# Optimization experiments

Hardware: AMD Instinct MI355X
Metric: run time of the kernel (lower is better)

The kernel has to match this reference:

```python
import jax, jax.numpy as jnp
import numpy as np
from jax import lax

B, C, H, W = 8, 128, 64, 64


def conv1x1(x, w):
    # x: [B, Cin, H, W], w: [Cout, Cin] (1x1 conv, no bias)
    return jnp.einsum('oc,bchw->bohw', w, x)


def maxpool2x2(x):
    # 2x2 max pool, stride 2, NCHW
    return lax.reduce_window(x, -jnp.inf, lax.max, (1, 1, 2, 2), (1, 1, 2, 2), 'VALID')


def setup_inputs() -> dict:
    key = jax.random.key(0)
    ks = jax.random.split(key, 5)
    c8, c2 = C // 8, C // 2
    inputs = jax.random.normal(ks[0], (B, C, H, W), dtype=jnp.float32)
    w_theta = jax.random.normal(ks[1], (c8, C), dtype=jnp.float32) * (1.0 / np.sqrt(C))
    w_phi = jax.random.normal(ks[2], (c8, C), dtype=jnp.float32) * (1.0 / np.sqrt(C))
    w_g = jax.random.normal(ks[3], (c2, C), dtype=jnp.float32) * (1.0 / np.sqrt(C))
    w_o = jax.random.normal(ks[4], (C, c2), dtype=jnp.float32) * (1.0 / np.sqrt(c2))
    gamma = jnp.float32(0.1)  # nonzero so attention branch contributes
    return {"inputs": inputs, "w_theta": w_theta, "w_phi": w_phi,
            "w_g": w_g, "w_o": w_o, "gamma": gamma}


def reference(inputs, w_theta, w_phi, w_g, w_o, gamma):
    batch, c, h, w = inputs.shape
    c8, c2 = c // 8, c // 2
    theta = conv1x1(inputs, w_theta).reshape(batch, c8, h * w)            # [B, C/8, HW]
    phi = maxpool2x2(conv1x1(inputs, w_phi)).reshape(batch, c8, -1)       # [B, C/8, HW/4]
    g = maxpool2x2(conv1x1(inputs, w_g)).reshape(batch, c2, -1)           # [B, C/2, HW/4]
    # beta[b, i, j] = softmax_j( theta[b,:,i] . phi[b,:,j] )
    scores = jnp.einsum('bci,bcj->bij', theta, phi)                       # [B, HW, HW/4]
    beta = jax.nn.softmax(scores, axis=-1)
    o = jnp.einsum('bcj,bij->bci', g, beta).reshape(batch, c2, h, w)      # [B, C/2, H, W]
    o = conv1x1(o, w_o)                                                   # [B, C, H, W]
    return gamma * o + inputs
```

## Files before the change

kernel.cpp:

```cpp
#include <hip/hip_runtime.h>
#include <math.h>

#define HW 4096
#define SHIFT 12.0f

typedef __attribute__((ext_vector_type(4)))  short short4v;
typedef __attribute__((ext_vector_type(8)))  short short8;
typedef __attribute__((ext_vector_type(4)))  float f32x4;
typedef __attribute__((ext_vector_type(16))) float f32x16;
typedef __attribute__((ext_vector_type(4)))  int   int4v;

#define MFMA16 __builtin_amdgcn_mfma_f32_16x16x32_bf16
#define MFMA32 __builtin_amdgcn_mfma_f32_32x32x16_bf16

__device__ inline short f2b(float f) {
    union { float f; unsigned u; } v; v.f = f;
    unsigned r = v.u + 0x7fffu + ((v.u >> 16) & 1u);
    return (short)(r >> 16);
}
__device__ inline int pk2(float a, float b) {
    return (int)((unsigned)(unsigned short)f2b(a) |
                 ((unsigned)(unsigned short)f2b(b) << 16));
}
__device__ inline short8 ld8(const float* p) {
    f32x4 a = *(const f32x4*)p;
    f32x4 b = *(const f32x4*)(p + 4);
    short8 r;
    r[0] = f2b(a.x); r[1] = f2b(a.y); r[2] = f2b(a.z); r[3] = f2b(a.w);
    r[4] = f2b(b.x); r[5] = f2b(b.y); r[6] = f2b(b.z); r[7] = f2b(b.w);
    return r;
}
__device__ inline float max4(float a, float b, float c, float d) {
    return fmaxf(fmaxf(a, b), fmaxf(c, d));
}

__global__ __launch_bounds__(256) void conv_pool(
    const float* __restrict__ x, const float* __restrict__ wt,
    const float* __restrict__ wp, const float* __restrict__ wg,
    short* __restrict__ theta_t, short* __restrict__ phi_t,
    short* __restrict__ g_blk)
{
    __shared__ __align__(16) short xl[128 * 68];
    const int tid = threadIdx.x;
    const int w = tid >> 6, lane = tid & 63, l15 = lane & 15, lg = (lane >> 4) & 3;
    const int bid = blockIdx.x;
    const int b = bid >> 6, ri = bid & 63, rp = ri >> 1, h = ri & 1;
    const float* xb = x + (size_t)b * 128 * HW + rp * 128 + h * 32;

    for (int it = 0; it < 8; it++) {
        int idx = it * 256 + tid;
        int c = idx >> 4, q = idx & 15;
        int px4 = q * 4, r = px4 >> 5, col4 = px4 & 31;
        f32x4 v = *(const f32x4*)(xb + (size_t)c * HW + r * 64 + col4);
        short4v sv = { f2b(v.x), f2b(v.y), f2b(v.z), f2b(v.w) };
        *(short4v*)(xl + c * 68 + px4) = sv;
    }
    __syncthreads();

    const int p = w & 1, csbase = (w >> 1) * 3;
    f32x4 acc[2][3];
#pragma unroll
    for (int cc = 0; cc < 2; cc++)
#pragma unroll
        for (int cl = 0; cl < 3; cl++) acc[cc][cl] = (f32x4){0.f, 0.f, 0.f, 0.f};

#pragma unroll
    for (int ks = 0; ks < 4; ks++) {
        short8 a[2];
#pragma unroll
        for (int cc = 0; cc < 2; cc++) {
            int px = (p + 2 * cc) * 16 + l15;
#pragma unroll
            for (int q = 0; q < 8; q++)
                a[cc][q] = xl[(ks * 32 + lg * 8 + q) * 68 + px];
        }
#pragma unroll
        for (int csl = 0; csl < 3; csl++) {
            int cs = csbase + csl;
            const float* wrow;
            if (cs == 0)      wrow = wt + l15 * 128;
            else if (cs == 1) wrow = wp + l15 * 128;
            else              wrow = wg + ((cs - 2) * 16 + l15) * 128;
            short8 bf = ld8(wrow + ks * 32 + lg * 8);
            acc[0][csl] = MFMA16(a[0], bf, acc[0][csl], 0, 0, 0);
            acc[1][csl] = MFMA16(a[1], bf, acc[1][csl], 0, 0, 0);
        }
    }

    const size_t pixb = (size_t)b * 4096 + rp * 128 + h * 32 + p * 16;
#pragma unroll
    for (int csl = 0; csl < 3; csl++) {
        int cs = csbase + csl;
        if (cs == 0) {
#pragma unroll
            for (int cc = 0; cc < 2; cc++)
#pragma unroll
                for (int r = 0; r < 4; r++)
                    theta_t[(pixb + cc * 64 + lg * 4 + r) * 16 + l15] =
                        f2b(acc[cc][csl][r]);
        } else if (cs == 1) {
#pragma unroll
            for (int h2 = 0; h2 < 2; h2++) {
                float m = max4(acc[0][csl][2 * h2], acc[0][csl][2 * h2 + 1],
                               acc[1][csl][2 * h2], acc[1][csl][2 * h2 + 1]);
                int j = rp * 32 + h * 16 + p * 8 + lg * 2 + h2;
                phi_t[((size_t)b * 1024 + j) * 16 + l15] = f2b(m);
            }
        } else {
            int gcrow = (cs - 2) * 16 + l15;
            float m0 = max4(acc[0][csl][0], acc[0][csl][1], acc[1][csl][0], acc[1][csl][1]);
            float m1 = max4(acc[0][csl][2], acc[0][csl][3], acc[1][csl][2], acc[1][csl][3]);
            int jb = rp * 2 + h, jl = p * 8 + lg * 2;
            *(int*)(g_blk + (((size_t)b * 64 + jb) * 64 + gcrow) * 16 + jl) = pk2(m0, m1);
        }
    }
}

__global__ __launch_bounds__(256) void attn_k(
    const float* __restrict__ x, const short* __restrict__ theta_t,
    const short* __restrict__ phi_t, const short* __restrict__ g_blk,
    const float* __restrict__ wo, const float* __restrict__ gamma_p,
    float* __restrict__ out)
{
    __shared__ float lds[4 * 2 * 16 * 64 + 4 * 64];
    const int tid = threadIdx.x;
    const int w = tid >> 6, lane = tid & 63, l31 = lane & 31, lam = lane >> 5;
    const int b = blockIdx.x >> 7, i0 = (blockIdx.x & 127) << 5;
    const int i = i0 + l31;

    short8 tb = *(const short8*)(theta_t + ((size_t)b * 4096 + i) * 16 + lam * 8);

    f32x16 acc0, acc1, z16;
#pragma unroll
    for (int r = 0; r < 16; r++) { acc0[r] = 0.f; acc1[r] = 0.f; z16[r] = 0.f; }
    float rs = 0.f;

    for (int t = 0; t < 4; t++) {
        const int jt = w * 4 + t;
        f32x16 s0, s1;
        {
            short8 pa0 = *(const short8*)(phi_t + ((size_t)b * 1024 + jt * 64 + l31) * 16 + lam * 8);
            short8 pa1 = *(const short8*)(phi_t + ((size_t)b * 1024 + jt * 64 + 32 + l31) * 16 + lam * 8);
            s0 = MFMA32(pa0, tb, z16, 0, 0, 0);
            s1 = MFMA32(pa1, tb, z16, 0, 0, 0);
        }
        int W[16], X[16];
#pragma unroll
        for (int jk = 0; jk < 2; jk++)
#pragma unroll
            for (int rg = 0; rg < 4; rg++)
#pragma unroll
                for (int h = 0; h < 2; h++) {
                    float p0 = __expf((jk ? s1 : s0)[rg * 4 + 2 * h]     - SHIFT);
                    float p1 = __expf((jk ? s1 : s0)[rg * 4 + 2 * h + 1] - SHIFT);
                    rs += p0 + p1;
                    W[jk * 8 + rg * 2 + h] = pk2(p0, p1);
                }
#pragma unroll
        for (int k = 0; k < 16; k++) X[k] = __shfl_xor(W[k], 32, 64);

#pragma unroll
        for (int ck = 0; ck < 4; ck++) {
            const int cb2 = (ck >> 1) * 8 + (ck & 1) * 4;
            int4v pi;
            pi.x = lam ? X[cb2 + 2] : W[cb2];
            pi.y = lam ? X[cb2 + 3] : W[cb2 + 1];
            pi.z = lam ? W[cb2 + 2] : X[cb2];
            pi.w = lam ? W[cb2 + 3] : X[cb2 + 1];
            short8 pb = __builtin_bit_cast(short8, pi);
            const short* gp = g_blk + (((size_t)b * 64 + jt * 4 + ck) * 64) * 16;
            short8 ga0 = *(const short8*)(gp + (l31)      * 16 + lam * 8);
            short8 ga1 = *(const short8*)(gp + (32 + l31) * 16 + lam * 8);
            acc0 = MFMA32(ga0, pb, acc0, 0, 0, 0);
            acc1 = MFMA32(ga1, pb, acc1, 0, 0, 0);
        }
    }

    rs += __shfl_xor(rs, 32, 64);

#pragma unroll
    for (int reg = 0; reg < 16; reg++) {
        lds[((w * 2 + 0) * 16 + reg) * 64 + lane] = acc0[reg];
        lds[((w * 2 + 1) * 16 + reg) * 64 + lane] = acc1[reg];
    }
    lds[8192 + w * 64 + lane] = rs;
    __syncthreads();

    float o[32];
#pragma unroll
    for (int cs2 = 0; cs2 < 2; cs2++)
#pragma unroll
        for (int reg = 0; reg < 16; reg++)
            o[cs2 * 16 + reg] =
                (lds[((0 * 2 + cs2) * 16 + reg) * 64 + lane] +
                 lds[((1 * 2 + cs2) * 16 + reg) * 64 + lane]) +
                (lds[((2 * 2 + cs2) * 16 + reg) * 64 + lane] +
                 lds[((3 * 2 + cs2) * 16 + reg) * 64 + lane]);
    float lf = (lds[8192 + 0 * 64 + lane] + lds[8192 + 1 * 64 + lane]) +
               (lds[8192 + 2 * 64 + lane] + lds[8192 + 3 * 64 + lane]);
    float rinv = 1.0f / lf;
#pragma unroll
    for (int k = 0; k < 32; k++) o[k] *= rinv;

    int Wo[16], Xo[16];
#pragma unroll
    for (int cs2 = 0; cs2 < 2; cs2++)
#pragma unroll
        for (int rg = 0; rg < 4; rg++)
#pragma unroll
            for (int h = 0; h < 2; h++)
                Wo[cs2 * 8 + rg * 2 + h] =
                    pk2(o[cs2 * 16 + rg * 4 + 2 * h], o[cs2 * 16 + rg * 4 + 2 * h + 1]);
#pragma unroll
    for (int k = 0; k < 16; k++) Xo[k] = __shfl_xor(Wo[k], 32, 64);

    const float gam = gamma_p[0];
    f32x16 oc;
#pragma unroll
    for (int r = 0; r < 16; r++) oc[r] = 0.f;
#pragma unroll
    for (int kc = 0; kc < 4; kc++) {
        const int cb2 = (kc >> 1) * 8 + (kc & 1) * 4;
        int4v pi;
        pi.x = lam ? Xo[cb2 + 2] : Wo[cb2];
        pi.y = lam ? Xo[cb2 + 3] : Wo[cb2 + 1];
        pi.z = lam ? Wo[cb2 + 2] : Xo[cb2];
        pi.w = lam ? Wo[cb2 + 3] : Xo[cb2 + 1];
        short8 ob = __builtin_bit_cast(short8, pi);
        short8 wa = ld8(wo + (size_t)(w * 32 + l31) * 64 + kc * 16 + lam * 8);
        oc = MFMA32(wa, ob, oc, 0, 0, 0);
    }
#pragma unroll
    for (int reg = 0; reg < 16; reg++) {
        int co = w * 32 + (reg & 3) + 8 * (reg >> 2) + 4 * lam;
        size_t idx = ((size_t)b * 128 + co) * HW + i0 + l31;
        out[idx] = gam * oc[reg] + x[idx];
    }
}

extern "C" void kernel_launch(void* const* d_in, const int* in_sizes, int n_in,
                              void* d_out, int out_size, void* d_ws, size_t ws_size,
                              hipStream_t stream)
{
    const float* x     = (const float*)d_in[0];
    const float* wt    = (const float*)d_in[1];
    const float* wp    = (const float*)d_in[2];
    const float* wg    = (const float*)d_in[3];
    const float* wo    = (const float*)d_in[4];
    const float* gamma = (const float*)d_in[5];
    float* out = (float*)d_out;

    char* ws = (char*)d_ws;
    short* theta_t = (short*)(ws + 0);
    short* phi_t   = (short*)(ws + 1048576);
    short* g_blk   = (short*)(ws + 1310720);

    conv_pool<<<512,  256, 0, stream>>>(x, wt, wp, wg, theta_t, phi_t, g_blk);
    attn_k   <<<1024, 256, 0, stream>>>(x, theta_t, phi_t, g_blk, wo, gamma, out);
}
```

Before: 102.9 us.

## Pre-convert weights to bf16 and use hardware pack and permlane swap instructions

Adds a small kernel that converts all four weight matrices to bf16 once per call, so the conv and attention kernels load bf16 weights directly instead of converting floats per lane. The software bf16 rounding is replaced with the v_cvt_pk_bf16_f32 instruction, and the xor-32 shuffles plus lane selects are replaced with v_permlane32_swap. The softmax shift is folded into the MFMA accumulator initial value, which removes a subtract per exponential. This costs an extra kernel launch and a workspace buffer for the converted weights.

```diff
diff --git a/kernel.cpp b/kernel.cpp
--- a/kernel.cpp
+++ b/kernel.cpp
@@ -6,9 +6,10 @@
 
 typedef __attribute__((ext_vector_type(4)))  short short4v;
 typedef __attribute__((ext_vector_type(8)))  short short8;
+typedef __attribute__((ext_vector_type(2)))  int   int2v;
+typedef __attribute__((ext_vector_type(4)))  int   int4v;
 typedef __attribute__((ext_vector_type(4)))  float f32x4;
 typedef __attribute__((ext_vector_type(16))) float f32x16;
-typedef __attribute__((ext_vector_type(4)))  int   int4v;
 
 #define MFMA16 __builtin_amdgcn_mfma_f32_16x16x32_bf16
 #define MFMA32 __builtin_amdgcn_mfma_f32_32x32x16_bf16
@@ -18,25 +19,36 @@
     unsigned r = v.u + 0x7fffu + ((v.u >> 16) & 1u);
     return (short)(r >> 16);
 }
-__device__ inline int pk2(float a, float b) {
-    return (int)((unsigned)(unsigned short)f2b(a) |
-                 ((unsigned)(unsigned short)f2b(b) << 16));
-}
-__device__ inline short8 ld8(const float* p) {
-    f32x4 a = *(const f32x4*)p;
-    f32x4 b = *(const f32x4*)(p + 4);
-    short8 r;
-    r[0] = f2b(a.x); r[1] = f2b(a.y); r[2] = f2b(a.z); r[3] = f2b(a.w);
-    r[4] = f2b(b.x); r[5] = f2b(b.y); r[6] = f2b(b.z); r[7] = f2b(b.w);
+__device__ inline int cvtpk(float lo, float hi) {
+    int r;
+    asm("v_cvt_pk_bf16_f32 %0, %1, %2" : "=v"(r) : "v"(lo), "v"(hi));
     return r;
+}
+__device__ inline void plswap(int& a, int& b) {
+    asm("v_permlane32_swap_b32 %0, %1" : "+v"(a), "+v"(b));
 }
 __device__ inline float max4(float a, float b, float c, float d) {
     return fmaxf(fmaxf(a, b), fmaxf(c, d));
 }
 
+__global__ __launch_bounds__(256) void wconv(
+    const float* __restrict__ wt, const float* __restrict__ wp,
+    const float* __restrict__ wg, const float* __restrict__ wo,
+    short* __restrict__ wb)
+{
+    int idx = (blockIdx.x * 256 + threadIdx.x) * 4;
+    const float* src;
+    if (idx < 2048)       src = wt + idx;
+    else if (idx < 4096)  src = wp + (idx - 2048);
+    else if (idx < 12288) src = wg + (idx - 4096);
+    else                  src = wo + (idx - 12288);
+    f32x4 v = *(const f32x4*)src;
+    int2v o; o.x = cvtpk(v.x, v.y); o.y = cvtpk(v.z, v.w);
+    *(int2v*)(wb + idx) = o;
+}
+
 __global__ __launch_bounds__(256) void conv_pool(
-    const float* __restrict__ x, const float* __restrict__ wt,
-    const float* __restrict__ wp, const float* __restrict__ wg,
+    const float* __restrict__ x, const short* __restrict__ wb,
     short* __restrict__ theta_t, short* __restrict__ phi_t,
     short* __restrict__ g_blk)
 {
@@ -52,12 +64,15 @@
         int c = idx >> 4, q = idx & 15;
         int px4 = q * 4, r = px4 >> 5, col4 = px4 & 31;
         f32x4 v = *(const f32x4*)(xb + (size_t)c * HW + r * 64 + col4);
-        short4v sv = { f2b(v.x), f2b(v.y), f2b(v.z), f2b(v.w) };
-        *(short4v*)(xl + c * 68 + px4) = sv;
+        int2v sv; sv.x = cvtpk(v.x, v.y); sv.y = cvtpk(v.z, v.w);
+        *(int2v*)(xl + c * 68 + px4) = sv;
     }
     __syncthreads();
 
     const int p = w & 1, csbase = (w >> 1) * 3;
+    const short* wb_t = wb;
+    const short* wb_p = wb + 2048;
+    const short* wb_g = wb + 4096;
     f32x4 acc[2][3];
 #pragma unroll
     for (int cc = 0; cc < 2; cc++)
@@ -77,11 +92,11 @@
 #pragma unroll
         for (int csl = 0; csl < 3; csl++) {
             int cs = csbase + csl;
-            const float* wrow;
-            if (cs == 0)      wrow = wt + l15 * 128;
-            else if (cs == 1) wrow = wp + l15 * 128;
-            else              wrow = wg + ((cs - 2) * 16 + l15) * 128;
-            short8 bf = ld8(wrow + ks * 32 + lg * 8);
+            const short* wrow;
+            if (cs == 0)      wrow = wb_t + l15 * 128;
+            else if (cs == 1) wrow = wb_p + l15 * 128;
+            else              wrow = wb_g + ((cs - 2) * 16 + l15) * 128;
+            short8 bf = *(const short8*)(wrow + ks * 32 + lg * 8);
             acc[0][csl] = MFMA16(a[0], bf, acc[0][csl], 0, 0, 0);
             acc[1][csl] = MFMA16(a[1], bf, acc[1][csl], 0, 0, 0);
         }
@@ -111,7 +126,7 @@
             float m0 = max4(acc[0][csl][0], acc[0][csl][1], acc[1][csl][0], acc[1][csl][1]);
             float m1 = max4(acc[0][csl][2], acc[0][csl][3], acc[1][csl][2], acc[1][csl][3]);
             int jb = rp * 2 + h, jl = p * 8 + lg * 2;
-            *(int*)(g_blk + (((size_t)b * 64 + jb) * 64 + gcrow) * 16 + jl) = pk2(m0, m1);
+            *(int*)(g_blk + (((size_t)b * 64 + jb) * 64 + gcrow) * 16 + jl) = cvtpk(m0, m1);
         }
     }
 }
@@ -119,7 +134,7 @@
 __global__ __launch_bounds__(256) void attn_k(
     const float* __restrict__ x, const short* __restrict__ theta_t,
     const short* __restrict__ phi_t, const short* __restrict__ g_blk,
-    const float* __restrict__ wo, const float* __restrict__ gamma_p,
+    const short* __restrict__ wo_b, const float* __restrict__ gamma_p,
     float* __restrict__ out)
 {
     __shared__ float lds[4 * 2 * 16 * 64 + 4 * 64];
@@ -132,7 +147,7 @@
 
     f32x16 acc0, acc1, z16;
 #pragma unroll
-    for (int r = 0; r < 16; r++) { acc0[r] = 0.f; acc1[r] = 0.f; z16[r] = 0.f; }
+    for (int r = 0; r < 16; r++) { acc0[r] = 0.f; acc1[r] = 0.f; z16[r] = -SHIFT; }
     float rs = 0.f;
 
     for (int t = 0; t < 4; t++) {
@@ -144,29 +159,26 @@
             s0 = MFMA32(pa0, tb, z16, 0, 0, 0);
             s1 = MFMA32(pa1, tb, z16, 0, 0, 0);
         }
-        int W[16], X[16];
+        int W[16];
 #pragma unroll
         for (int jk = 0; jk < 2; jk++)
 #pragma unroll
             for (int rg = 0; rg < 4; rg++)
 #pragma unroll
                 for (int h = 0; h < 2; h++) {
-                    float p0 = __expf((jk ? s1 : s0)[rg * 4 + 2 * h]     - SHIFT);
-                    float p1 = __expf((jk ? s1 : s0)[rg * 4 + 2 * h + 1] - SHIFT);
+                    float p0 = __expf((jk ? s1 : s0)[rg * 4 + 2 * h]);
+                    float p1 = __expf((jk ? s1 : s0)[rg * 4 + 2 * h + 1]);
                     rs += p0 + p1;
-                    W[jk * 8 + rg * 2 + h] = pk2(p0, p1);
+                    W[jk * 8 + rg * 2 + h] = cvtpk(p0, p1);
                 }
-#pragma unroll
-        for (int k = 0; k < 16; k++) X[k] = __shfl_xor(W[k], 32, 64);
 
 #pragma unroll
         for (int ck = 0; ck < 4; ck++) {
             const int cb2 = (ck >> 1) * 8 + (ck & 1) * 4;
-            int4v pi;
-            pi.x = lam ? X[cb2 + 2] : W[cb2];
-            pi.y = lam ? X[cb2 + 3] : W[cb2 + 1];
-            pi.z = lam ? W[cb2 + 2] : X[cb2];
-            pi.w = lam ? W[cb2 + 3] : X[cb2 + 1];
+            int a0 = W[cb2], a1 = W[cb2 + 1], a2 = W[cb2 + 2], a3 = W[cb2 + 3];
+            plswap(a0, a2);
+            plswap(a1, a3);
+            int4v pi; pi.x = a0; pi.y = a1; pi.z = a2; pi.w = a3;
             short8 pb = __builtin_bit_cast(short8, pi);
             const short* gp = g_blk + (((size_t)b * 64 + jt * 4 + ck) * 64) * 16;
             short8 ga0 = *(const short8*)(gp + (l31)      * 16 + lam * 8);
@@ -202,7 +214,7 @@
 #pragma unroll
     for (int k = 0; k < 32; k++) o[k] *= rinv;
 
-    int Wo[16], Xo[16];
+    int Wo[16];
 #pragma unroll
     for (int cs2 = 0; cs2 < 2; cs2++)
 #pragma unroll
@@ -210,9 +222,7 @@
 #pragma unroll
             for (int h = 0; h < 2; h++)
                 Wo[cs2 * 8 + rg * 2 + h] =
-                    pk2(o[cs2 * 16 + rg * 4 + 2 * h], o[cs2 * 16 + rg * 4 + 2 * h + 1]);
-#pragma unroll
-    for (int k = 0; k < 16; k++) Xo[k] = __shfl_xor(Wo[k], 32, 64);
+                    cvtpk(o[cs2 * 16 + rg * 4 + 2 * h], o[cs2 * 16 + rg * 4 + 2 * h + 1]);
 
     const float gam = gamma_p[0];
     f32x16 oc;
@@ -221,13 +231,12 @@
 #pragma unroll
     for (int kc = 0; kc < 4; kc++) {
         const int cb2 = (kc >> 1) * 8 + (kc & 1) * 4;
-        int4v pi;
-        pi.x = lam ? Xo[cb2 + 2] : Wo[cb2];
-        pi.y = lam ? Xo[cb2 + 3] : Wo[cb2 + 1];
-        pi.z = lam ? Wo[cb2 + 2] : Xo[cb2];
-        pi.w = lam ? Wo[cb2 + 3] : Xo[cb2 + 1];
+        int a0 = Wo[cb2], a1 = Wo[cb2 + 1], a2 = Wo[cb2 + 2], a3 = Wo[cb2 + 3];
+        plswap(a0, a2);
+        plswap(a1, a3);
+        int4v pi; pi.x = a0; pi.y = a1; pi.z = a2; pi.w = a3;
         short8 ob = __builtin_bit_cast(short8, pi);
-        short8 wa = ld8(wo + (size_t)(w * 32 + l31) * 64 + kc * 16 + lam * 8);
+        short8 wa = *(const short8*)(wo_b + (size_t)(w * 32 + l31) * 64 + kc * 16 + lam * 8);
         oc = MFMA32(wa, ob, oc, 0, 0, 0);
     }
 #pragma unroll
@@ -254,7 +263,9 @@
     short* theta_t = (short*)(ws + 0);
     short* phi_t   = (short*)(ws + 1048576);
     short* g_blk   = (short*)(ws + 1310720);
-
-    conv_pool<<<512,  256, 0, stream>>>(x, wt, wp, wg, theta_t, phi_t, g_blk);
-    attn_k   <<<1024, 256, 0, stream>>>(x, theta_t, phi_t, g_blk, wo, gamma, out);
-}
+    short* wb      = (short*)(ws + 2359296);
+
+    wconv    <<<20,   256, 0, stream>>>(wt, wp, wg, wo, wb);
+    conv_pool<<<512,  256, 0, stream>>>(x, wb, theta_t, phi_t, g_blk);
+    attn_k   <<<1024, 256, 0, stream>>>(x, theta_t, phi_t, g_blk, wb + 12288, gamma, out);
+}
```

Result: faster. 97.11 us (-5.6%).
